# Kernel optimization log

Measured on AMD Instinct MI355X. Metric: run time of the kernel, lower is better.

## Reference

```python
import jax, jax.numpy as jnp
import numpy as np

L, B, D = 8, 32, 1280  # layers, batch, padded block-diagonal width (64 wires x 20)


def setup_inputs() -> dict:
    key = jax.random.key(0)
    k1, k2, k3, k4 = jax.random.split(key, 4)
    x = jax.random.normal(k1, (B, D), dtype=jnp.float32)
    # scale ~ glorot so activations stay O(1) across 8 layers
    weights = jax.random.normal(k2, (L, B, D, D), dtype=jnp.float32) * 0.02
    biases = jax.random.normal(k3, (L, B, D), dtype=jnp.float32)
    masks = jax.random.randint(k4, (L, B, D), 0, 2, dtype=jnp.int32)
    return {"x": x, "weights": weights, "biases": biases, "masks": masks}


def reference(x, weights, biases, masks):
    # Sequentially apply L batched dense layers:
    #   out = einsum('bi,bij->bj', h, W) + b ; relu applied only where mask==1
    def step(h, wbm):
        w, b, m = wbm  # w:[B,D,D], b:[B,D], m:[B,D]
        out = jnp.einsum('bi,bij->bj', h, w) + b
        out = jnp.where(m.astype(bool), jax.nn.relu(out), out)
        return out, None

    h, _ = jax.lax.scan(step, x, (weights, biases, masks))
    return h
```

## Files before the change

kernel.cpp:

```cpp
#include <hip/hip_runtime.h>
#include <hip/hip_bf16.h>

constexpr int L = 8;
constexpr int B = 32;
constexpr int D = 1280;

constexpr int JT = 64;
constexpr int ISPLIT = 4;
constexpr int BLOCK = JT * ISPLIT;
constexpr int ICHUNK = D / ISPLIT;

__global__ __launch_bounds__(BLOCK) void layer_kernel(
    const float* __restrict__ h_in,
    const float* __restrict__ W,
    const float* __restrict__ bias,
    const int*   __restrict__ mask,
    float*       __restrict__ h_out)
{
    const int b  = blockIdx.y;
    const int j0 = blockIdx.x * JT;
    const int t  = threadIdx.x;
    const int jj = t & (JT - 1);
    const int iq = t >> 6;
    const int j  = j0 + jj;

    __shared__ float hs[D];
    __shared__ float partial[BLOCK];

    for (int i = t; i < D; i += BLOCK) hs[i] = h_in[b * D + i];
    __syncthreads();

    const float* w = W + (size_t)b * D * D + j;
    const int i_beg = iq * ICHUNK;
    float acc = 0.f;
#pragma unroll 8
    for (int i = i_beg; i < i_beg + ICHUNK; ++i) {
        acc = fmaf(hs[i], w[(size_t)i * D], acc);
    }

    partial[t] = acc;
    __syncthreads();

    if (t < JT) {
        float s = partial[t] + partial[t + 64] + partial[t + 128] + partial[t + 192];
        const int idx = b * D + j0 + t;
        s += bias[idx];
        if (mask[idx]) s = fmaxf(s, 0.f);
        h_out[idx] = s;
    }
}

extern "C" void kernel_launch(void* const* d_in, const int* in_sizes, int n_in,
                              void* d_out, int out_size, void* d_ws, size_t ws_size,
                              hipStream_t stream) {
    const float* x       = (const float*)d_in[0];
    const float* weights = (const float*)d_in[1];
    const float* biases  = (const float*)d_in[2];
    const int*   masks   = (const int*)  d_in[3];
    float* out = (float*)d_out;

    float* ws0 = (float*)d_ws;
    float* ws1 = ws0 + B * D;

    dim3 grid(D / JT, B);
    dim3 block(BLOCK);

    const float* hin = x;
    for (int l = 0; l < L; ++l) {
        float* hout = (l == L - 1) ? out : ((l & 1) ? ws1 : ws0);
        layer_kernel<<<grid, block, 0, stream>>>(
            hin,
            weights + (size_t)l * B * D * D,
            biases  + (size_t)l * B * D,
            masks   + (size_t)l * B * D,
            hout);
        hin = hout;
    }
}
```

Measured before the change: 307.5 us.

## Use persistent blocks with atomic work stealing and weight prefetch

Replaces the fixed 20x32 grid with 512 statically assigned blocks that then pull the remaining tiles from a per-layer atomic counter. Each block also issues loads for its first 16 weight rows before staging h into shared memory, so that global latency overlaps the staging. The goal is better load balance and less tail effect in the memory-bound weight stream. The cost is extra atomics and barriers, plus a memset launch per call.

After: 378.9 us. 23.2% more time.

```diff
diff --git a/kernel.cpp b/kernel.cpp
--- a/kernel.cpp
+++ b/kernel.cpp
@@ -9,44 +9,89 @@
 constexpr int ISPLIT = 4;
 constexpr int BLOCK = JT * ISPLIT;
 constexpr int ICHUNK = D / ISPLIT;
+constexpr int NBB = D / JT;
+constexpr int NT = NBB * B;
+constexpr int NSTATIC = 512;
+constexpr int PF = 16;
 
 __global__ __launch_bounds__(BLOCK) void layer_kernel(
-    const float* __restrict__ h_in,
+    const float* __restrict__ hin,
     const float* __restrict__ W,
     const float* __restrict__ bias,
     const int*   __restrict__ mask,
-    float*       __restrict__ h_out)
+    float*       __restrict__ hout,
+    int*         __restrict__ steal)
 {
-    const int b  = blockIdx.y;
-    const int j0 = blockIdx.x * JT;
     const int t  = threadIdx.x;
     const int jj = t & (JT - 1);
     const int iq = t >> 6;
-    const int j  = j0 + jj;
+    const int i_beg = iq * ICHUNK;
 
     __shared__ float hs[D];
     __shared__ float partial[BLOCK];
+    __shared__ int   stile;
 
-    for (int i = t; i < D; i += BLOCK) hs[i] = h_in[b * D + i];
-    __syncthreads();
+    {
+        const int tile = blockIdx.x;
+        const int b = tile / NBB, j0 = (tile % NBB) * JT;
+        const float* w = W + (size_t)b * D * D + j0 + jj;
 
-    const float* w = W + (size_t)b * D * D + j;
-    const int i_beg = iq * ICHUNK;
-    float acc = 0.f;
-#pragma unroll 8
-    for (int i = i_beg; i < i_beg + ICHUNK; ++i) {
-        acc = fmaf(hs[i], w[(size_t)i * D], acc);
+        float pf[PF];
+#pragma unroll
+        for (int k = 0; k < PF; ++k) pf[k] = w[(size_t)(i_beg + k) * D];
+
+        const float4* src = (const float4*)(hin + b * D);
+        float4* dst = (float4*)hs;
+        for (int k = t; k < D / 4; k += BLOCK) dst[k] = src[k];
+        __syncthreads();
+
+        float acc = 0.f;
+#pragma unroll
+        for (int k = 0; k < PF; ++k) acc = fmaf(hs[i_beg + k], pf[k], acc);
+#pragma unroll 16
+        for (int i = i_beg + PF; i < i_beg + ICHUNK; ++i)
+            acc = fmaf(hs[i], w[(size_t)i * D], acc);
+
+        partial[t] = acc;
+        __syncthreads();
+        if (t < JT) {
+            float s = partial[t] + partial[t + 64] + partial[t + 128] + partial[t + 192];
+            const int idx = b * D + j0 + t;
+            s += bias[idx];
+            if (mask[idx]) s = fmaxf(s, 0.f);
+            hout[idx] = s;
+        }
     }
 
-    partial[t] = acc;
-    __syncthreads();
+    for (;;) {
+        __syncthreads();
+        if (t == 0) stile = NSTATIC + atomicAdd(steal, 1);
+        __syncthreads();
+        const int tile = stile;
+        if (tile >= NT) break;
 
-    if (t < JT) {
-        float s = partial[t] + partial[t + 64] + partial[t + 128] + partial[t + 192];
-        const int idx = b * D + j0 + t;
-        s += bias[idx];
-        if (mask[idx]) s = fmaxf(s, 0.f);
-        h_out[idx] = s;
+        const int b = tile / NBB, j0 = (tile % NBB) * JT;
+
+        const float4* src = (const float4*)(hin + b * D);
+        float4* dst = (float4*)hs;
+        for (int k = t; k < D / 4; k += BLOCK) dst[k] = src[k];
+        __syncthreads();
+
+        const float* w = W + (size_t)b * D * D + j0 + jj;
+        float acc = 0.f;
+#pragma unroll 16
+        for (int i = i_beg; i < i_beg + ICHUNK; ++i)
+            acc = fmaf(hs[i], w[(size_t)i * D], acc);
+
+        partial[t] = acc;
+        __syncthreads();
+        if (t < JT) {
+            float s = partial[t] + partial[t + 64] + partial[t + 128] + partial[t + 192];
+            const int idx = b * D + j0 + t;
+            s += bias[idx];
+            if (mask[idx]) s = fmaxf(s, 0.f);
+            hout[idx] = s;
+        }
     }
 }
 
@@ -61,8 +106,11 @@
 
     float* ws0 = (float*)d_ws;
     float* ws1 = ws0 + B * D;
+    int*   cnt = (int*)(ws1 + B * D);
 
-    dim3 grid(D / JT, B);
+    hipMemsetAsync(cnt, 0, L * sizeof(int), stream);
+
+    dim3 grid(NSTATIC);
     dim3 block(BLOCK);
 
     const float* hin = x;
@@ -73,7 +121,8 @@
             weights + (size_t)l * B * D * D,
             biases  + (size_t)l * B * D,
             masks   + (size_t)l * B * D,
-            hout);
+            hout,
+            cnt + l);
         hin = hout;
     }
 }
```

## Split layers along input rows with float4 row streaming and atomic reduction

Applied to the files above, without the earlier changes.

Each layer kernel now gives each block a chunk of 80 input rows of W, and each wave streams contiguous W rows as float4 loads, so every thread accumulates 20 output columns in registers. Before, each thread read one strided column. Partial sums are combined across waves in shared memory and then across blocks with atomicAdd into a zeroed workspace. The next layer applies bias-free relu/mask when it loads its input, and a small finish kernel applies the last mask. This trades fully coalesced wide weight reads for a memset, extra atomic traffic, nondeterministic summation order, a higher register count, and a dependence on workspace size, with the old path kept as a fallback.

Result: slower. 316.1 us (+2.8%).

```diff
diff --git a/kernel.cpp b/kernel.cpp
--- a/kernel.cpp
+++ b/kernel.cpp
@@ -5,17 +5,103 @@
 constexpr int B = 32;
 constexpr int D = 1280;
 
+constexpr int NIC   = 16;
+constexpr int ROWS  = D / NIC;
+constexpr int BLOCK = 256;
+constexpr int WAVES = 4;
+constexpr int RPW   = ROWS / WAVES;
+constexpr int NQ    = D / 256;
+
+__global__ __launch_bounds__(BLOCK) void layer_seq_kernel(
+    const float* __restrict__ x,
+    const float* __restrict__ Wl,
+    const float* __restrict__ bias_l,
+    const float* __restrict__ accprev,
+    const int*   __restrict__ maskprev,
+    float*       __restrict__ accout)
+{
+    const int b    = blockIdx.y;
+    const int ic   = blockIdx.x;
+    const int i0   = ic * ROWS;
+    const int t    = threadIdx.x;
+    const int w    = t >> 6;
+    const int lane = t & 63;
+
+    __shared__ float hs[ROWS];
+    __shared__ float p[WAVES][D];
+
+    if (t < ROWS / 4) {
+        const int ii = 4 * t;
+        float4 v;
+        if (accprev == nullptr) {
+            v = *(const float4*)(x + (size_t)b * D + i0 + ii);
+        } else {
+            v = *(const float4*)(accprev + (size_t)b * D + i0 + ii);
+            const int4 m = *(const int4*)(maskprev + (size_t)b * D + i0 + ii);
+            if (m.x) v.x = fmaxf(v.x, 0.f);
+            if (m.y) v.y = fmaxf(v.y, 0.f);
+            if (m.z) v.z = fmaxf(v.z, 0.f);
+            if (m.w) v.w = fmaxf(v.w, 0.f);
+        }
+        *(float4*)(hs + ii) = v;
+    }
+    __syncthreads();
+
+    float4 acc[NQ];
+#pragma unroll
+    for (int q = 0; q < NQ; ++q) acc[q] = make_float4(0.f, 0.f, 0.f, 0.f);
+
+    const float4* wrow = (const float4*)(Wl + ((size_t)b * D + i0 + w * RPW) * D);
+#pragma unroll 4
+    for (int r = 0; r < RPW; ++r) {
+        const float hv = hs[w * RPW + r];
+        const float4* row = wrow + (size_t)r * (D / 4);
+#pragma unroll
+        for (int q = 0; q < NQ; ++q) {
+            const float4 wv = row[q * 64 + lane];
+            acc[q].x = fmaf(hv, wv.x, acc[q].x);
+            acc[q].y = fmaf(hv, wv.y, acc[q].y);
+            acc[q].z = fmaf(hv, wv.z, acc[q].z);
+            acc[q].w = fmaf(hv, wv.w, acc[q].w);
+        }
+    }
+
+#pragma unroll
+    for (int q = 0; q < NQ; ++q)
+        *(float4*)(&p[w][q * 256 + 4 * lane]) = acc[q];
+    __syncthreads();
+
+    const float* bb = bias_l + (size_t)b * D;
+#pragma unroll
+    for (int k = 0; k < NQ; ++k) {
+        const int j = t + 256 * k;
+        float s = p[0][j] + p[1][j] + p[2][j] + p[3][j];
+        if (ic == 0) s += bb[j];
+        atomicAdd(accout + (size_t)b * D + j, s);
+    }
+}
+
+__global__ __launch_bounds__(256) void finish_kernel(
+    const float* __restrict__ acc7, const int* __restrict__ mask7,
+    float* __restrict__ out)
+{
+    const int idx = blockIdx.x * 256 + threadIdx.x;
+    if (idx < B * D) {
+        float v = acc7[idx];
+        if (mask7[idx]) v = fmaxf(v, 0.f);
+        out[idx] = v;
+    }
+}
+
 constexpr int JT = 64;
 constexpr int ISPLIT = 4;
-constexpr int BLOCK = JT * ISPLIT;
+constexpr int FBLOCK = JT * ISPLIT;
 constexpr int ICHUNK = D / ISPLIT;
 
-__global__ __launch_bounds__(BLOCK) void layer_kernel(
-    const float* __restrict__ h_in,
-    const float* __restrict__ W,
-    const float* __restrict__ bias,
-    const int*   __restrict__ mask,
-    float*       __restrict__ h_out)
+__global__ __launch_bounds__(FBLOCK) void layer_kernel(
+    const float* __restrict__ h_in, const float* __restrict__ W,
+    const float* __restrict__ bias, const int* __restrict__ mask,
+    float* __restrict__ h_out)
 {
     const int b  = blockIdx.y;
     const int j0 = blockIdx.x * JT;
@@ -25,18 +111,17 @@
     const int j  = j0 + jj;
 
     __shared__ float hs[D];
-    __shared__ float partial[BLOCK];
+    __shared__ float partial[FBLOCK];
 
-    for (int i = t; i < D; i += BLOCK) hs[i] = h_in[b * D + i];
+    for (int i = t; i < D; i += FBLOCK) hs[i] = h_in[b * D + i];
     __syncthreads();
 
     const float* w = W + (size_t)b * D * D + j;
     const int i_beg = iq * ICHUNK;
     float acc = 0.f;
 #pragma unroll 8
-    for (int i = i_beg; i < i_beg + ICHUNK; ++i) {
+    for (int i = i_beg; i < i_beg + ICHUNK; ++i)
         acc = fmaf(hs[i], w[(size_t)i * D], acc);
-    }
 
     partial[t] = acc;
     __syncthreads();
@@ -59,21 +144,38 @@
     const int*   masks   = (const int*)  d_in[3];
     float* out = (float*)d_out;
 
-    float* ws0 = (float*)d_ws;
-    float* ws1 = ws0 + B * D;
+    const size_t need = (size_t)L * B * D * sizeof(float);
 
-    dim3 grid(D / JT, B);
-    dim3 block(BLOCK);
+    if (ws_size >= need) {
+        float* acc = (float*)d_ws;
+        hipMemsetAsync(acc, 0, need, stream);
 
-    const float* hin = x;
-    for (int l = 0; l < L; ++l) {
-        float* hout = (l == L - 1) ? out : ((l & 1) ? ws1 : ws0);
-        layer_kernel<<<grid, block, 0, stream>>>(
-            hin,
-            weights + (size_t)l * B * D * D,
-            biases  + (size_t)l * B * D,
-            masks   + (size_t)l * B * D,
-            hout);
-        hin = hout;
+        dim3 grid(NIC, B);
+        for (int l = 0; l < L; ++l) {
+            layer_seq_kernel<<<grid, BLOCK, 0, stream>>>(
+                x,
+                weights + (size_t)l * B * D * D,
+                biases  + (size_t)l * B * D,
+                l ? acc + (size_t)(l - 1) * B * D : nullptr,
+                l ? masks + (size_t)(l - 1) * B * D : nullptr,
+                acc + (size_t)l * B * D);
+        }
+        finish_kernel<<<(B * D + 255) / 256, 256, 0, stream>>>(
+            acc + (size_t)(L - 1) * B * D, masks + (size_t)(L - 1) * B * D, out);
+    } else {
+        float* ws0 = (float*)d_ws;
+        float* ws1 = ws0 + B * D;
+        dim3 grid(D / JT, B);
+        const float* hin = x;
+        for (int l = 0; l < L; ++l) {
+            float* hout = (l == L - 1) ? out : ((l & 1) ? ws1 : ws0);
+            layer_kernel<<<grid, FBLOCK, 0, stream>>>(
+                hin,
+                weights + (size_t)l * B * D * D,
+                biases  + (size_t)l * B * D,
+                masks   + (size_t)l * B * D,
+                hout);
+            hin = hout;
+        }
     }
 }
```
